# Kernel optimization log

Measured on AMD Instinct MI355X. Metric: run time of the kernel, lower is better.

The kernel has to match this reference:

```python
import jax, jax.numpy as jnp
import numpy as np

D = 1024
H = 16


def setup_inputs() -> dict:
    key = jax.random.key(0)
    ks = jax.random.split(key, 5)
    s = 1.0 / np.sqrt(D)
    x = jax.random.normal(ks[0], (4, 1024, D), dtype=jnp.float32)
    W_qkv = jax.random.normal(ks[1], (D, 3 * D), dtype=jnp.float32) * s
    b_qkv = jnp.zeros((3 * D,), dtype=jnp.float32)
    W_out = jax.random.normal(ks[2], (D, D), dtype=jnp.float32) * s
    b_out = jnp.zeros((D,), dtype=jnp.float32)
    return {"x": x, "W_qkv": W_qkv, "b_qkv": b_qkv, "W_out": W_out, "b_out": b_out}


def reference(x, W_qkv, b_qkv, W_out, b_out):
    bs, ns, d = x.shape
    dh = d // H
    scale = 1.0 / np.sqrt(dh)
    qkv = x @ W_qkv + b_qkv                      # [B,S,3D]
    qkv = qkv.reshape(bs, ns, 3, H, dh)
    q, k, v = qkv[:, :, 0], qkv[:, :, 1], qkv[:, :, 2]  # [B,S,H,dh]
    # attention scores [B,H,S,S]
    attn = jnp.einsum('bqhd,bkhd->bhqk', q, k) * scale
    attn = jax.nn.softmax(attn, axis=-1)
    out = jnp.einsum('bhqk,bkhd->bqhd', attn, v)  # [B,S,H,dh]
    out = out.reshape(bs, ns, d)
    return out @ W_out + b_out
```

## Files before the change

kernel.cpp:

```cpp
#include <hip/hip_runtime.h>
#include <hip/hip_bf16.h>
#include <cstdint>

typedef __bf16 bf16x8 __attribute__((ext_vector_type(8)));
typedef float f32x4 __attribute__((ext_vector_type(4)));
typedef unsigned short ushort8 __attribute__((ext_vector_type(8)));

__device__ __forceinline__ unsigned short f2b(float f) {
  __bf16 h = (__bf16)f;
  return __builtin_bit_cast(unsigned short, h);
}

__device__ __forceinline__ void gload_lds16(const void* g, void* l) {
  __builtin_amdgcn_global_load_lds(
      (__attribute__((address_space(1))) void*)g,
      (__attribute__((address_space(3))) void*)l,
      16, 0, 0);
}

__device__ __forceinline__ void barrier_pinned() {
  __builtin_amdgcn_sched_barrier(0);
  __builtin_amdgcn_s_barrier();
  __builtin_amdgcn_sched_barrier(0);
}

__global__ void prep(const float* __restrict__ x, unsigned short* __restrict__ xb,
                     const float* __restrict__ Wqkv, unsigned short* __restrict__ wqkvT,
                     const float* __restrict__ Wout, unsigned short* __restrict__ woutT) {
  const int bid = blockIdx.x, t = threadIdx.x;
  if (bid < 2048) {
    int i = (bid * 256 + t) * 8;
    float4 f0 = *(const float4*)&x[i];
    float4 f1 = *(const float4*)&x[i + 4];
    ushort8 u;
    u[0] = f2b(f0.x); u[1] = f2b(f0.y); u[2] = f2b(f0.z); u[3] = f2b(f0.w);
    u[4] = f2b(f1.x); u[5] = f2b(f1.y); u[6] = f2b(f1.z); u[7] = f2b(f1.w);
    *(ushort8*)&xb[i] = u;
    return;
  }
  __shared__ float tile[64][65];
  const float* in; unsigned short* out; int R, C, c0, r0;
  if (bid < 2816) {
    int i = bid - 2048; in = Wqkv; out = wqkvT; R = 1024; C = 3072;
    c0 = (i % 48) * 64; r0 = (i / 48) * 64;
  } else {
    int i = bid - 2816; in = Wout; out = woutT; R = 1024; C = 1024;
    c0 = (i & 15) * 64; r0 = (i >> 4) * 64;
  }
  #pragma unroll
  for (int rd = 0; rd < 4; rd++) {
    int row = rd * 16 + (t >> 4);
    int col = (t & 15) * 4;
    float4 f = *(const float4*)&in[(size_t)(r0 + row) * C + c0 + col];
    tile[row][col] = f.x; tile[row][col + 1] = f.y;
    tile[row][col + 2] = f.z; tile[row][col + 3] = f.w;
  }
  __syncthreads();
  #pragma unroll
  for (int rd = 0; rd < 4; rd++) {
    int item = rd * 256 + t;
    int cc = item >> 4, rr = (item & 15) * 4;
    ushort4 u = make_ushort4(f2b(tile[rr][cc]), f2b(tile[rr + 1][cc]),
                             f2b(tile[rr + 2][cc]), f2b(tile[rr + 3][cc]));
    *(ushort4*)&out[(size_t)(c0 + cc) * R + r0 + rr] = u;
  }
}

__global__ __launch_bounds__(512, 2)
void gemm256_8ph(const unsigned short* __restrict__ Ag,
                 const unsigned short* __restrict__ Bt,
                 const float* __restrict__ bias,
                 unsigned short* __restrict__ C,
                 unsigned short* __restrict__ vt,
                 int M, int N, int K) {
  __shared__ __align__(16) unsigned short sA[2][256 * 64];
  __shared__ __align__(16) unsigned short sB[2][256 * 64];
  const int t = threadIdx.x;
  const int wid = t >> 6, lane = t & 63;
  const int ln = lane & 15, lq = lane >> 4;
  const int wm = wid >> 2, wn = wid & 3;

  const int nwg = gridDim.x;
  const int cpx = nwg >> 3;
  const int wg = (blockIdx.x & 7) * cpx + (blockIdx.x >> 3);
  const int nbx = N >> 8;
  const int m0 = (wg / nbx) * 256, n0 = (wg % nbx) * 256;

  f32x4 acc[8][4];
  #pragma unroll
  for (int i = 0; i < 8; i++)
    #pragma unroll
    for (int j = 0; j < 4; j++) acc[i][j] = (f32x4){0.f, 0.f, 0.f, 0.f};

  auto stageA = [&](int buf, int kt, int h) {
    #pragma unroll
    for (int g = 0; g < 2; g++) {
      int idx = g * 512 + t;
      int row = h * 128 + (idx >> 3), ch = idx & 7;
      gload_lds16(Ag + (size_t)(m0 + row) * K + kt * 64 + ((ch ^ (row & 7)) * 8),
                  &sA[buf][h * 8192 + idx * 8]);
    }
  };
  auto stageB = [&](int buf, int kt, int h) {
    #pragma unroll
    for (int g = 0; g < 2; g++) {
      int idx = g * 512 + t;
      int row = h * 128 + (idx >> 3), ch = idx & 7;
      gload_lds16(Bt + (size_t)(n0 + row) * K + kt * 64 + ((ch ^ (row & 7)) * 8),
                  &sB[buf][h * 8192 + idx * 8]);
    }
  };

  const int nt = K >> 6;

  stageB(0, 0, 0); stageB(0, 0, 1);
  stageA(0, 0, 0); stageA(0, 0, 1);
  stageB(1, 1, 0); stageB(1, 1, 1);
  stageA(1, 1, 0); stageA(1, 1, 1);
  asm volatile("s_waitcnt vmcnt(8)" ::: "memory");
  barrier_pinned();

  bf16x8 af[8], bf01[4], bf23[4];

  for (int T = 0; T < nt; ++T) {
    const int cur = T & 1;

    #pragma unroll
    for (int i = 0; i < 4; i++)
      #pragma unroll
      for (int kk = 0; kk < 2; kk++)
        af[i * 2 + kk] = *(const bf16x8*)&sA[cur][(wm * 128 + i * 16 + ln) * 64 +
                                                  ((kk * 4 + lq) ^ (ln & 7)) * 8];
    #pragma unroll
    for (int j = 0; j < 2; j++)
      #pragma unroll
      for (int kk = 0; kk < 2; kk++)
        bf01[j * 2 + kk] = *(const bf16x8*)&sB[cur][(wn * 64 + j * 16 + ln) * 64 +
                                                    ((kk * 4 + lq) ^ (ln & 7)) * 8];
    barrier_pinned();
    asm volatile("s_waitcnt lgkmcnt(0)" ::: "memory");
    __builtin_amdgcn_sched_barrier(0);
    #pragma unroll
    for (int i = 0; i < 4; i++)
      #pragma unroll
      for (int j = 0; j < 2; j++)
        #pragma unroll
        for (int kk = 0; kk < 2; kk++)
          acc[i][j] = __builtin_amdgcn_mfma_f32_16x16x32_bf16(af[i * 2 + kk], bf01[j * 2 + kk], acc[i][j], 0, 0, 0);
    barrier_pinned();

    #pragma unroll
    for (int j = 0; j < 2; j++)
      #pragma unroll
      for (int kk = 0; kk < 2; kk++)
        bf23[j * 2 + kk] = *(const bf16x8*)&sB[cur][(wn * 64 + (2 + j) * 16 + ln) * 64 +
                                                    ((kk * 4 + lq) ^ (ln & 7)) * 8];
    barrier_pinned();
    asm volatile("s_waitcnt lgkmcnt(0)" ::: "memory");
    __builtin_amdgcn_sched_barrier(0);
    #pragma unroll
    for (int i = 0; i < 4; i++)
      #pragma unroll
      for (int j = 0; j < 2; j++)
        #pragma unroll
        for (int kk = 0; kk < 2; kk++)
          acc[i][2 + j] = __builtin_amdgcn_mfma_f32_16x16x32_bf16(af[i * 2 + kk], bf23[j * 2 + kk], acc[i][2 + j], 0, 0, 0);
    barrier_pinned();

    #pragma unroll
    for (int i = 0; i < 4; i++)
      #pragma unroll
      for (int kk = 0; kk < 2; kk++)
        af[i * 2 + kk] = *(const bf16x8*)&sA[cur][(wm * 128 + (4 + i) * 16 + ln) * 64 +
                                                  ((kk * 4 + lq) ^ (ln & 7)) * 8];
    if (T + 2 < nt) { stageB(cur, T + 2, 0); stageB(cur, T + 2, 1); }
    barrier_pinned();
    asm volatile("s_waitcnt lgkmcnt(0)" ::: "memory");
    __builtin_amdgcn_sched_barrier(0);
    #pragma unroll
    for (int i = 0; i < 4; i++)
      #pragma unroll
      for (int j = 0; j < 2; j++)
        #pragma unroll
        for (int kk = 0; kk < 2; kk++)
          acc[4 + i][j] = __builtin_amdgcn_mfma_f32_16x16x32_bf16(af[i * 2 + kk], bf01[j * 2 + kk], acc[4 + i][j], 0, 0, 0);
    barrier_pinned();

    if (T + 2 < nt) { stageA(cur, T + 2, 0); stageA(cur, T + 2, 1); }
    if (T + 2 < nt)  asm volatile("s_waitcnt vmcnt(8)" ::: "memory");
    else             asm volatile("s_waitcnt vmcnt(0)" ::: "memory");
    barrier_pinned();
    asm volatile("s_waitcnt lgkmcnt(0)" ::: "memory");
    __builtin_amdgcn_sched_barrier(0);
    #pragma unroll
    for (int i = 0; i < 4; i++)
      #pragma unroll
      for (int j = 0; j < 2; j++)
        #pragma unroll
        for (int kk = 0; kk < 2; kk++)
          acc[4 + i][2 + j] = __builtin_amdgcn_mfma_f32_16x16x32_bf16(af[i * 2 + kk], bf23[j * 2 + kk], acc[4 + i][2 + j], 0, 0, 0);
    barrier_pinned();
  }

  if (vt == nullptr || n0 < 2048) {
    #pragma unroll
    for (int m = 0; m < 8; m++) {
      #pragma unroll
      for (int n = 0; n < 4; n++) {
        int col = n0 + wn * 64 + n * 16 + ln;
        float bv = bias[col];
        #pragma unroll
        for (int r = 0; r < 4; r++) {
          int row = m0 + wm * 128 + m * 16 + lq * 4 + r;
          C[(size_t)row * N + col] = f2b(acc[m][n][r] + bv);
        }
      }
    }
  } else {
    #pragma unroll
    for (int n = 0; n < 4; n++) {
      int col = n0 + wn * 64 + n * 16 + ln;
      int rel = col - 2048;
      int hh = rel >> 6, dd = rel & 63;
      float bv = bias[col];
      #pragma unroll
      for (int m = 0; m < 8; m++) {
        int grow = m0 + wm * 128 + m * 16 + lq * 4;
        int bb = grow >> 10, ss = grow & 1023;
        ushort4 u = make_ushort4(f2b(acc[m][n][0] + bv), f2b(acc[m][n][1] + bv),
                                 f2b(acc[m][n][2] + bv), f2b(acc[m][n][3] + bv));
        *(ushort4*)&vt[((size_t)((bb * 16 + hh) * 64 + dd) << 10) + ss] = u;
      }
    }
  }
}

template <int OUT_F32>
__global__ __launch_bounds__(256, 2)
void gemm_bt(const unsigned short* __restrict__ A,
             const unsigned short* __restrict__ Bt,
             const float* __restrict__ bias, void* __restrict__ C,
             int M, int N, int K) {
  __shared__ __align__(16) unsigned short sA[2][128 * 32];
  __shared__ __align__(16) unsigned short sB[2][128 * 32];
  const int t = threadIdx.x;
  const int w = t >> 6, lane = t & 63;
  const int ln = lane & 15, lq = lane >> 4;
  const int wr = w >> 1, wc = w & 1;
  const int wg = (blockIdx.x & 7) * (gridDim.x >> 3) + (blockIdx.x >> 3);
  const int nbx = N >> 7;
  const int m0 = (wg / nbx) * 128, n0 = (wg % nbx) * 128;

  f32x4 acc[4][4];
  #pragma unroll
  for (int i = 0; i < 4; i++)
    #pragma unroll
    for (int j = 0; j < 4; j++) acc[i][j] = (f32x4){0.f, 0.f, 0.f, 0.f};

  auto stage = [&](int buf, int k0) {
    #pragma unroll
    for (int i = 0; i < 2; ++i) {
      int idx = i * 256 + t;
      int row = idx >> 2;
      int cb = (idx & 3) * 8;
      gload_lds16(A + (size_t)(m0 + row) * K + k0 + cb, &sA[buf][idx * 8]);
    }
    #pragma unroll
    for (int i = 0; i < 2; ++i) {
      int idx = i * 256 + t;
      int row = idx >> 2;
      int cb = (idx & 3) * 8;
      gload_lds16(Bt + (size_t)(n0 + row) * K + k0 + cb, &sB[buf][idx * 8]);
    }
  };

  stage(0, 0);
  asm volatile("s_waitcnt vmcnt(0)" ::: "memory");
  __builtin_amdgcn_s_barrier();
  __builtin_amdgcn_sched_barrier(0);

  const int nk = K >> 5;
  for (int ki = 0; ki < nk; ++ki) {
    const int cur = ki & 1;
    if (ki + 1 < nk) stage(cur ^ 1, (ki + 1) << 5);

    bf16x8 af[4], bfr[4];
    #pragma unroll
    for (int m = 0; m < 4; m++)
      af[m] = *(const bf16x8*)&sA[cur][(wr * 64 + m * 16 + ln) * 32 + lq * 8];
    #pragma unroll
    for (int n = 0; n < 4; n++)
      bfr[n] = *(const bf16x8*)&sB[cur][(wc * 64 + n * 16 + ln) * 32 + lq * 8];
    #pragma unroll
    for (int m = 0; m < 4; m++)
      #pragma unroll
      for (int n = 0; n < 4; n++)
        acc[m][n] = __builtin_amdgcn_mfma_f32_16x16x32_bf16(af[m], bfr[n], acc[m][n], 0, 0, 0);

    asm volatile("s_waitcnt vmcnt(0)" ::: "memory");
    __builtin_amdgcn_s_barrier();
    __builtin_amdgcn_sched_barrier(0);
  }

  #pragma unroll
  for (int m = 0; m < 4; m++) {
    #pragma unroll
    for (int n = 0; n < 4; n++) {
      int col = n0 + wc * 64 + n * 16 + ln;
      float bv = bias[col];
      #pragma unroll
      for (int r = 0; r < 4; r++) {
        int row = m0 + wr * 64 + m * 16 + lq * 4 + r;
        float v = acc[m][n][r] + bv;
        if (OUT_F32)
          ((float*)C)[(size_t)row * N + col] = v;
        else
          ((unsigned short*)C)[(size_t)row * N + col] = f2b(v);
      }
    }
  }
}

__global__ __launch_bounds__(256, 4)
void attn_fwd(const unsigned short* __restrict__ qkv,
              const unsigned short* __restrict__ vt,
              unsigned short* __restrict__ aout) {
  const int wg = ((blockIdx.x & 7) << 7) + (blockIdx.x >> 3);
  const int bh = wg >> 4, q0 = (wg & 15) * 64;
  const int b = bh >> 4, h = bh & 15;
  __shared__ __align__(16) unsigned short sB[4][64 * 64];
  __shared__ __align__(16) unsigned short sP[4][16 * 64];
  const int t = threadIdx.x;
  const int w = t >> 6, lane = t & 63;
  const int ln = lane & 15, lq = lane >> 4;
  const float K2 = 0.125f * 1.44269504f;
  const float CEXP = 48.f * K2;

  const size_t qbase = (size_t)(b * 1024 + q0) * 3072 + h * 64;
  const size_t kbase = (size_t)(b * 1024) * 3072 + 1024 + h * 64;
  const size_t vbase = (size_t)((b * 16 + h) * 64) * 1024;

  const unsigned short* gk[2];
  const unsigned short* gv[2];
  int ldst[2];
  #pragma unroll
  for (int i = 0; i < 2; i++) {
    int idx = i * 256 + t;
    int row = idx >> 3, ch = idx & 7;
    int sw = (ch ^ (row & 7)) * 8;
    gk[i] = qkv + kbase + (size_t)(64 + row) * 3072 + sw;
    gv[i] = vt + vbase + (size_t)row * 1024 + 64 + sw;
    ldst[i] = idx * 8;
  }

  #pragma unroll
  for (int i = 0; i < 2; i++) {
    int idx = i * 256 + t;
    int row = idx >> 3, ch = idx & 7;
    int sw = (ch ^ (row & 7)) * 8;
    gload_lds16(qkv + qbase + (size_t)row * 3072 + sw, &sB[0][idx * 8]);
    gload_lds16(qkv + kbase + (size_t)row * 3072 + sw, &sB[1][idx * 8]);
    gload_lds16(vt + vbase + (size_t)row * 1024 + sw, &sB[2][idx * 8]);
  }
  __syncthreads();
  bf16x8 qf[2];
  #pragma unroll
  for (int c = 0; c < 2; c++) {
    int row = w * 16 + ln;
    qf[c] = *(const bf16x8*)&sB[0][row * 64 + ((c * 4 + lq) ^ (ln & 7)) * 8];
  }
  __syncthreads();

  f32x4 o[4];
  float lsum = 0.f;
  #pragma unroll
  for (int n = 0; n < 4; n++) o[n] = (f32x4){0.f, 0.f, 0.f, 0.f};

  for (int kt = 0; kt < 16; ++kt) {
    const unsigned short* kb = sB[(kt & 1) ? 3 : 1];
    const unsigned short* vb = sB[(kt & 1) ? 0 : 2];
    if (kt < 15) {
      unsigned short* kn = sB[(kt & 1) ? 1 : 3];
      unsigned short* vn = sB[(kt & 1) ? 2 : 0];
      #pragma unroll
      for (int i = 0; i < 2; i++) {
        gload_lds16(gk[i], &kn[ldst[i]]);
        gload_lds16(gv[i], &vn[ldst[i]]);
        gk[i] += 64 * 3072;
        gv[i] += 64;
      }
    }

    f32x4 st[4];
    #pragma unroll
    for (int kc = 0; kc < 4; kc++) {
      int krow = kc * 16 + ln;
      bf16x8 k0f = *(const bf16x8*)&kb[krow * 64 + ((0 + lq) ^ (ln & 7)) * 8];
      bf16x8 k1f = *(const bf16x8*)&kb[krow * 64 + ((4 + lq) ^ (ln & 7)) * 8];
      st[kc] = __builtin_amdgcn_mfma_f32_16x16x32_bf16(k0f, qf[0], (f32x4){0.f, 0.f, 0.f, 0.f}, 0, 0, 0);
      st[kc] = __builtin_amdgcn_mfma_f32_16x16x32_bf16(k1f, qf[1], st[kc], 0, 0, 0);
    }

    float xv[4][4];
    float ts = 0.f;
    #pragma unroll
    for (int kc = 0; kc < 4; kc++) {
      #pragma unroll
      for (int r = 0; r < 4; r++) {
        xv[kc][r] = exp2f(fmaf(st[kc][r], K2, -CEXP));
        ts += xv[kc][r];
      }
    }
    ts += __shfl_xor(ts, 16);
    ts += __shfl_xor(ts, 32);
    lsum += ts;

    unsigned char* pb = (unsigned char*)sP[w];
    #pragma unroll
    for (int kc = 0; kc < 4; kc++) {
      ushort4 u = make_ushort4(f2b(xv[kc][0]), f2b(xv[kc][1]),
                               f2b(xv[kc][2]), f2b(xv[kc][3]));
      int boff = (kc * 32 + lq * 8) ^ ((ln & 7) << 4);
      *(ushort4*)(pb + ln * 128 + boff) = u;
    }

    #pragma unroll
    for (int c2 = 0; c2 < 2; c2++) {
      bf16x8 pa = *(const bf16x8*)&sP[w][ln * 64 + ((c2 * 4 + lq) ^ (ln & 7)) * 8];
      #pragma unroll
      for (int n = 0; n < 4; n++) {
        int vrow = n * 16 + ln;
        bf16x8 vf = *(const bf16x8*)&vb[vrow * 64 + ((c2 * 4 + lq) ^ (ln & 7)) * 8];
        o[n] = __builtin_amdgcn_mfma_f32_16x16x32_bf16(pa, vf, o[n], 0, 0, 0);
      }
    }

    asm volatile("s_waitcnt vmcnt(0)" ::: "memory");
    __builtin_amdgcn_s_barrier();
    __builtin_amdgcn_sched_barrier(0);
  }

  float linv[4];
  #pragma unroll
  for (int r = 0; r < 4; r++)
    linv[r] = 1.f / __shfl(lsum, (lane & 48) | (lq * 4 + r));
  #pragma unroll
  for (int n = 0; n < 4; n++) {
    #pragma unroll
    for (int r = 0; r < 4; r++) {
      int row = q0 + w * 16 + lq * 4 + r;
      int col = h * 64 + n * 16 + ln;
      aout[(size_t)(b * 1024 + row) * 1024 + col] = f2b(o[n][r] * linv[r]);
    }
  }
}

extern "C" void kernel_launch(void* const* d_in, const int* in_sizes, int n_in,
                              void* d_out, int out_size, void* d_ws, size_t ws_size,
                              hipStream_t stream) {
  const float* x = (const float*)d_in[0];
  const float* W_qkv = (const float*)d_in[1];
  const float* b_qkv = (const float*)d_in[2];
  const float* W_out = (const float*)d_in[3];
  const float* b_out = (const float*)d_in[4];
  float* out = (float*)d_out;

  char* ws = (char*)d_ws;
  unsigned short* xb    = (unsigned short*)(ws);
  unsigned short* wqkvT = (unsigned short*)(ws + 8388608);
  unsigned short* woutT = (unsigned short*)(ws + 14680064);
  unsigned short* qkv   = (unsigned short*)(ws + 16777216);
  unsigned short* vt    = (unsigned short*)(ws + 41943040);
  unsigned short* aout  = (unsigned short*)(ws + 50331648);
  if (ws_size < 58720256) return;

  prep<<<3072, 256, 0, stream>>>(x, xb, W_qkv, wqkvT, W_out, woutT);
  gemm256_8ph<<<192, 512, 0, stream>>>(xb, wqkvT, b_qkv, qkv, vt, 4096, 3072, 1024);
  attn_fwd<<<1024, 256, 0, stream>>>(qkv, vt, aout);
  gemm_bt<1><<<256, 256, 0, stream>>>(aout, woutT, b_out, out, 4096, 1024, 1024);
}
```

Measured before the change: 109.4 us.

## Replace 256x256 eight-phase QKV GEMM with simpler 128x128 double-buffered kernel

Swaps the QKV projection GEMM from a 256x256-tile, 512-thread kernel with an 8-phase interleaved LDS/MFMA schedule and XOR-swizzled LDS layout for a 128x128-tile, 256-thread kernel with K-step 32, plain double buffering and no swizzle. The grid grows from 192 to 768 workgroups, which gives better coverage across the CUs. In exchange, each tile reuses data less, barriers and global loads happen more often, and unswizzled LDS reads may hit bank conflicts.

Result: faster. 105.6 us, median of 2 (-3.5%).

```diff
diff --git a/kernel.cpp b/kernel.cpp
--- a/kernel.cpp
+++ b/kernel.cpp
@@ -16,12 +16,6 @@
       (__attribute__((address_space(1))) void*)g,
       (__attribute__((address_space(3))) void*)l,
       16, 0, 0);
-}
-
-__device__ __forceinline__ void barrier_pinned() {
-  __builtin_amdgcn_sched_barrier(0);
-  __builtin_amdgcn_s_barrier();
-  __builtin_amdgcn_sched_barrier(0);
 }
 
 __global__ void prep(const float* __restrict__ x, unsigned short* __restrict__ xb,
@@ -66,166 +60,93 @@
   }
 }
 
-__global__ __launch_bounds__(512, 2)
-void gemm256_8ph(const unsigned short* __restrict__ Ag,
-                 const unsigned short* __restrict__ Bt,
-                 const float* __restrict__ bias,
-                 unsigned short* __restrict__ C,
-                 unsigned short* __restrict__ vt,
-                 int M, int N, int K) {
-  __shared__ __align__(16) unsigned short sA[2][256 * 64];
-  __shared__ __align__(16) unsigned short sB[2][256 * 64];
+__global__ __launch_bounds__(256, 2)
+void gemm_qkv(const unsigned short* __restrict__ A,
+              const unsigned short* __restrict__ Bt,
+              const float* __restrict__ bias,
+              unsigned short* __restrict__ C,
+              unsigned short* __restrict__ vt,
+              int M, int N, int K) {
+  __shared__ __align__(16) unsigned short sA[2][128 * 32];
+  __shared__ __align__(16) unsigned short sB[2][128 * 32];
   const int t = threadIdx.x;
-  const int wid = t >> 6, lane = t & 63;
+  const int w = t >> 6, lane = t & 63;
   const int ln = lane & 15, lq = lane >> 4;
-  const int wm = wid >> 2, wn = wid & 3;
-
-  const int nwg = gridDim.x;
-  const int cpx = nwg >> 3;
-  const int wg = (blockIdx.x & 7) * cpx + (blockIdx.x >> 3);
-  const int nbx = N >> 8;
-  const int m0 = (wg / nbx) * 256, n0 = (wg % nbx) * 256;
-
-  f32x4 acc[8][4];
-  #pragma unroll
-  for (int i = 0; i < 8; i++)
+  const int wr = w >> 1, wc = w & 1;
+  const int wg = (blockIdx.x & 7) * (gridDim.x >> 3) + (blockIdx.x >> 3);
+  const int nbx = N >> 7;
+  const int m0 = (wg / nbx) * 128, n0 = (wg % nbx) * 128;
+
+  f32x4 acc[4][4];
+  #pragma unroll
+  for (int i = 0; i < 4; i++)
     #pragma unroll
     for (int j = 0; j < 4; j++) acc[i][j] = (f32x4){0.f, 0.f, 0.f, 0.f};
 
-  auto stageA = [&](int buf, int kt, int h) {
-    #pragma unroll
-    for (int g = 0; g < 2; g++) {
-      int idx = g * 512 + t;
-      int row = h * 128 + (idx >> 3), ch = idx & 7;
-      gload_lds16(Ag + (size_t)(m0 + row) * K + kt * 64 + ((ch ^ (row & 7)) * 8),
-                  &sA[buf][h * 8192 + idx * 8]);
+  auto stage = [&](int buf, int k0) {
+    #pragma unroll
+    for (int i = 0; i < 2; ++i) {
+      int idx = i * 256 + t;
+      int row = idx >> 2;
+      int cb = (idx & 3) * 8;
+      gload_lds16(A + (size_t)(m0 + row) * K + k0 + cb, &sA[buf][idx * 8]);
+    }
+    #pragma unroll
+    for (int i = 0; i < 2; ++i) {
+      int idx = i * 256 + t;
+      int row = idx >> 2;
+      int cb = (idx & 3) * 8;
+      gload_lds16(Bt + (size_t)(n0 + row) * K + k0 + cb, &sB[buf][idx * 8]);
     }
   };
-  auto stageB = [&](int buf, int kt, int h) {
-    #pragma unroll
-    for (int g = 0; g < 2; g++) {
-      int idx = g * 512 + t;
-      int row = h * 128 + (idx >> 3), ch = idx & 7;
-      gload_lds16(Bt + (size_t)(n0 + row) * K + kt * 64 + ((ch ^ (row & 7)) * 8),
-                  &sB[buf][h * 8192 + idx * 8]);
-    }
-  };
-
-  const int nt = K >> 6;
-
-  stageB(0, 0, 0); stageB(0, 0, 1);
-  stageA(0, 0, 0); stageA(0, 0, 1);
-  stageB(1, 1, 0); stageB(1, 1, 1);
-  stageA(1, 1, 0); stageA(1, 1, 1);
-  asm volatile("s_waitcnt vmcnt(8)" ::: "memory");
-  barrier_pinned();
-
-  bf16x8 af[8], bf01[4], bf23[4];
-
-  for (int T = 0; T < nt; ++T) {
-    const int cur = T & 1;
-
-    #pragma unroll
-    for (int i = 0; i < 4; i++)
-      #pragma unroll
-      for (int kk = 0; kk < 2; kk++)
-        af[i * 2 + kk] = *(const bf16x8*)&sA[cur][(wm * 128 + i * 16 + ln) * 64 +
-                                                  ((kk * 4 + lq) ^ (ln & 7)) * 8];
-    #pragma unroll
-    for (int j = 0; j < 2; j++)
-      #pragma unroll
-      for (int kk = 0; kk < 2; kk++)
-        bf01[j * 2 + kk] = *(const bf16x8*)&sB[cur][(wn * 64 + j * 16 + ln) * 64 +
-                                                    ((kk * 4 + lq) ^ (ln & 7)) * 8];
-    barrier_pinned();
-    asm volatile("s_waitcnt lgkmcnt(0)" ::: "memory");
+
+  stage(0, 0);
+  asm volatile("s_waitcnt vmcnt(0)" ::: "memory");
+  __builtin_amdgcn_s_barrier();
+  __builtin_amdgcn_sched_barrier(0);
+
+  const int nk = K >> 5;
+  for (int ki = 0; ki < nk; ++ki) {
+    const int cur = ki & 1;
+    if (ki + 1 < nk) stage(cur ^ 1, (ki + 1) << 5);
+
+    bf16x8 af[4], bfr[4];
+    #pragma unroll
+    for (int m = 0; m < 4; m++)
+      af[m] = *(const bf16x8*)&sA[cur][(wr * 64 + m * 16 + ln) * 32 + lq * 8];
+    #pragma unroll
+    for (int n = 0; n < 4; n++)
+      bfr[n] = *(const bf16x8*)&sB[cur][(wc * 64 + n * 16 + ln) * 32 + lq * 8];
+    #pragma unroll
+    for (int m = 0; m < 4; m++)
+      #pragma unroll
+      for (int n = 0; n < 4; n++)
+        acc[m][n] = __builtin_amdgcn_mfma_f32_16x16x32_bf16(af[m], bfr[n], acc[m][n], 0, 0, 0);
+
+    asm volatile("s_waitcnt vmcnt(0)" ::: "memory");
+    __builtin_amdgcn_s_barrier();
     __builtin_amdgcn_sched_barrier(0);
-    #pragma unroll
-    for (int i = 0; i < 4; i++)
-      #pragma unroll
-      for (int j = 0; j < 2; j++)
-        #pragma unroll
-        for (int kk = 0; kk < 2; kk++)
-          acc[i][j] = __builtin_amdgcn_mfma_f32_16x16x32_bf16(af[i * 2 + kk], bf01[j * 2 + kk], acc[i][j], 0, 0, 0);
-    barrier_pinned();
-
-    #pragma unroll
-    for (int j = 0; j < 2; j++)
-      #pragma unroll
-      for (int kk = 0; kk < 2; kk++)
-        bf23[j * 2 + kk] = *(const bf16x8*)&sB[cur][(wn * 64 + (2 + j) * 16 + ln) * 64 +
-                                                    ((kk * 4 + lq) ^ (ln & 7)) * 8];
-    barrier_pinned();
-    asm volatile("s_waitcnt lgkmcnt(0)" ::: "memory");
-    __builtin_amdgcn_sched_barrier(0);
-    #pragma unroll
-    for (int i = 0; i < 4; i++)
-      #pragma unroll
-      for (int j = 0; j < 2; j++)
-        #pragma unroll
-        for (int kk = 0; kk < 2; kk++)
-          acc[i][2 + j] = __builtin_amdgcn_mfma_f32_16x16x32_bf16(af[i * 2 + kk], bf23[j * 2 + kk], acc[i][2 + j], 0, 0, 0);
-    barrier_pinned();
-
-    #pragma unroll
-    for (int i = 0; i < 4; i++)
-      #pragma unroll
-      for (int kk = 0; kk < 2; kk++)
-        af[i * 2 + kk] = *(const bf16x8*)&sA[cur][(wm * 128 + (4 + i) * 16 + ln) * 64 +
-                                                  ((kk * 4 + lq) ^ (ln & 7)) * 8];
-    if (T + 2 < nt) { stageB(cur, T + 2, 0); stageB(cur, T + 2, 1); }
-    barrier_pinned();
-    asm volatile("s_waitcnt lgkmcnt(0)" ::: "memory");
-    __builtin_amdgcn_sched_barrier(0);
-    #pragma unroll
-    for (int i = 0; i < 4; i++)
-      #pragma unroll
-      for (int j = 0; j < 2; j++)
-        #pragma unroll
-        for (int kk = 0; kk < 2; kk++)
-          acc[4 + i][j] = __builtin_amdgcn_mfma_f32_16x16x32_bf16(af[i * 2 + kk], bf01[j * 2 + kk], acc[4 + i][j], 0, 0, 0);
-    barrier_pinned();
-
-    if (T + 2 < nt) { stageA(cur, T + 2, 0); stageA(cur, T + 2, 1); }
-    if (T + 2 < nt)  asm volatile("s_waitcnt vmcnt(8)" ::: "memory");
-    else             asm volatile("s_waitcnt vmcnt(0)" ::: "memory");
-    barrier_pinned();
-    asm volatile("s_waitcnt lgkmcnt(0)" ::: "memory");
-    __builtin_amdgcn_sched_barrier(0);
-    #pragma unroll
-    for (int i = 0; i < 4; i++)
-      #pragma unroll
-      for (int j = 0; j < 2; j++)
-        #pragma unroll
-        for (int kk = 0; kk < 2; kk++)
-          acc[4 + i][2 + j] = __builtin_amdgcn_mfma_f32_16x16x32_bf16(af[i * 2 + kk], bf23[j * 2 + kk], acc[4 + i][2 + j], 0, 0, 0);
-    barrier_pinned();
-  }
-
-  if (vt == nullptr || n0 < 2048) {
-    #pragma unroll
-    for (int m = 0; m < 8; m++) {
-      #pragma unroll
-      for (int n = 0; n < 4; n++) {
-        int col = n0 + wn * 64 + n * 16 + ln;
-        float bv = bias[col];
+  }
+
+  #pragma unroll
+  for (int n = 0; n < 4; n++) {
+    int col = n0 + wc * 64 + n * 16 + ln;
+    float bv = bias[col];
+    if (col < 2048) {
+      #pragma unroll
+      for (int m = 0; m < 4; m++) {
         #pragma unroll
         for (int r = 0; r < 4; r++) {
-          int row = m0 + wm * 128 + m * 16 + lq * 4 + r;
+          int row = m0 + wr * 64 + m * 16 + lq * 4 + r;
           C[(size_t)row * N + col] = f2b(acc[m][n][r] + bv);
         }
       }
-    }
-  } else {
-    #pragma unroll
-    for (int n = 0; n < 4; n++) {
-      int col = n0 + wn * 64 + n * 16 + ln;
+    } else {
       int rel = col - 2048;
       int hh = rel >> 6, dd = rel & 63;
-      float bv = bias[col];
-      #pragma unroll
-      for (int m = 0; m < 8; m++) {
-        int grow = m0 + wm * 128 + m * 16 + lq * 4;
+      #pragma unroll
+      for (int m = 0; m < 4; m++) {
+        int grow = m0 + wr * 64 + m * 16 + lq * 4;
         int bb = grow >> 10, ss = grow & 1023;
         ushort4 u = make_ushort4(f2b(acc[m][n][0] + bv), f2b(acc[m][n][1] + bv),
                                  f2b(acc[m][n][2] + bv), f2b(acc[m][n][3] + bv));
@@ -475,7 +396,7 @@
   if (ws_size < 58720256) return;
 
   prep<<<3072, 256, 0, stream>>>(x, xb, W_qkv, wqkvT, W_out, woutT);
-  gemm256_8ph<<<192, 512, 0, stream>>>(xb, wqkvT, b_qkv, qkv, vt, 4096, 3072, 1024);
+  gemm_qkv<<<768, 256, 0, stream>>>(xb, wqkvT, b_qkv, qkv, vt, 4096, 3072, 1024);
   attn_fwd<<<1024, 256, 0, stream>>>(qkv, vt, aout);
   gemm_bt<1><<<256, 256, 0, stream>>>(aout, woutT, b_out, out, 4096, 1024, 1024);
 }
```
